# Optimization experiments

Measured on AMD Instinct MI355X. Metric: run time of the kernel, lower is better.

## Reference

```python
import jax, jax.numpy as jnp
import numpy as np

B, N, C, W = 256, 4096, 16, 10
L = N - W + 1
EPS = 1e-5


def setup_inputs() -> dict:
    key = jax.random.key(0)
    ks = jax.random.split(key, 6)
    def lin(k, shape, fan_in):
        # mimic nn.Linear default init scale ~ U(-1/sqrt(fan), 1/sqrt(fan))
        b = 1.0 / np.sqrt(fan_in)
        return jax.random.uniform(k, shape, jnp.float32, -b, b)
    return {
        "x": jax.random.normal(ks[0], (B, N, C, 2), jnp.float32),
        "W_in_real": lin(ks[1], (C, L), L),      # per-channel input filter (real)
        "W_in_imag": lin(ks[2], (C, L), L),      # per-channel input filter (imag)
        "W_nl": lin(ks[3], (C, 2, 2 * C), 2 * C),  # per-channel Linear(2C -> 2)
        "W_out_real": lin(ks[4], (C, W), W),      # per-channel output filter (real)
        "W_out_imag": lin(ks[5], (C, W), W),      # per-channel output filter (imag)
        "gamma": jnp.ones((C,), jnp.float32),     # BatchNorm1d weight
        "beta": jnp.zeros((C,), jnp.float32),     # BatchNorm1d bias
    }


def _depthwise_valid(x_bcn, w_cl):
    # sliding dot-products f[:, c, id] = sum_l x[:, c, id+l] * w[c, l]
    # == depthwise 1D valid correlation: [B,C,N] * [C,L] -> [B,C,W]
    nC = w_cl.shape[0]
    return jax.lax.conv_general_dilated(
        x_bcn, w_cl[:, None, :], window_strides=(1,), padding='VALID',
        dimension_numbers=('NCH', 'OIH', 'NCH'), feature_group_count=nC)


def reference(x, W_in_real, W_in_imag, W_nl, W_out_real, W_out_imag, gamma, beta):
    xr = jnp.transpose(x[..., 0], (0, 2, 1))  # [B,C,N]
    xi = jnp.transpose(x[..., 1], (0, 2, 1))
    # stage 1: per-channel windowed filters + amplitude (|f|^2) scaling
    fr = jnp.transpose(_depthwise_valid(xr, W_in_real), (0, 2, 1))  # [B,W,C]
    fi = jnp.transpose(_depthwise_valid(xi, W_in_imag), (0, 2, 1))  # [B,W,C]
    amp = fr * fr + fi * fi
    fr = amp * fr
    fi = amp * fi
    # stage 2: per-channel nonlin Linear(2C -> 2) on cat([real, imag])
    tf = jnp.concatenate([fr, fi], axis=-1)            # [B,W,2C]
    nl = jnp.einsum('bwi,coi->bwco', tf, W_nl)         # [B,W,C,2]
    nr, ni = nl[..., 0], nl[..., 1]                    # [B,W,C]
    # stage 3: per-channel output filters over the out_window dim
    out_r = jnp.einsum('bwc,cw->bc', nr, W_out_real)   # [B,C]
    out_i = jnp.einsum('bwc,cw->bc', ni, W_out_imag)   # [B,C]
    out = jnp.stack([out_r, out_i], axis=-1)           # [B,C,2]
    # BatchNorm1d(n_channels) in training mode: stats over (batch, last) per channel
    mean = out.mean(axis=(0, 2), keepdims=True)
    var = out.var(axis=(0, 2), keepdims=True)
    return (out - mean) / jnp.sqrt(var + EPS) * gamma[None, :, None] + beta[None, :, None]
```

## Files before the change

### kernel.cpp

```cpp
#include <hip/hip_runtime.h>

#define BB 256
#define NN 4096
#define CC 16
#define WW 10
#define LL 4087
#define EPSF 1e-5f

__global__ __launch_bounds__(256) void pack_weights(const float* __restrict__ Wr,
                                                    const float* __restrict__ Wi,
                                                    float2* __restrict__ pk) {
    int tg = blockIdx.x * 256 + threadIdx.x;
    int n = tg >> 4, c = tg & 15;
    float2 v = make_float2(0.f, 0.f);
    if (n < LL) { v.x = Wr[c * LL + n]; v.y = Wi[c * LL + n]; }
    pk[tg] = v;
}

template <bool PK>
__global__ __launch_bounds__(512, 2) void fused_main(const float* __restrict__ x,
                                                     const float2* __restrict__ pk,
                                                     const float* __restrict__ Wr,
                                                     const float* __restrict__ Wi,
                                                     const float* __restrict__ Wnl,
                                                     const float* __restrict__ Wor,
                                                     const float* __restrict__ Woi,
                                                     float* __restrict__ outraw) {
    const int b = blockIdx.x;
    const int tid = threadIdx.x;
    const int tc = tid >> 4;
    const int c = tid & 15;
    const int n0 = tc * 128;

    const float2* __restrict__ x2 = (const float2*)x + (size_t)b * (NN * CC);

    float wr[16], wi[16];
    float fr[WW], fi[WW];
#pragma unroll
    for (int w = 0; w < WW; ++w) { fr[w] = 0.f; fi[w] = 0.f; }

#pragma unroll
    for (int i = 1; i <= 9; ++i) {
        const int m = n0 - i;
        float vr = 0.f, vi = 0.f;
        if (PK) {
            if (m >= 0) { const float2 t = pk[m * 16 + c]; vr = t.x; vi = t.y; }
        } else {
            const int mc = m < 0 ? 0 : m;
            const float a = Wr[c * LL + mc], q = Wi[c * LL + mc];
            vr = (m >= 0) ? a : 0.f;
            vi = (m >= 0) ? q : 0.f;
        }
        wr[16 - i] = vr;
        wi[16 - i] = vi;
    }

#pragma unroll 1
    for (int g = 0; g < 8; ++g) {
        const int nb = n0 + g * 16;
#pragma unroll
        for (int p = 0; p < 16; ++p) {
            const int n = nb + p;
            float vr, vi;
            if (PK) {
                const float2 t = pk[n * 16 + c];
                vr = t.x; vi = t.y;
            } else {
                const int nc2 = (n < LL) ? n : (LL - 1);
                const float a = Wr[c * LL + nc2], q = Wi[c * LL + nc2];
                vr = (n < LL) ? a : 0.f;
                vi = (n < LL) ? q : 0.f;
            }
            const float2 xv = x2[n * 16 + c];
            wr[p] = vr;
            wi[p] = vi;
#pragma unroll
            for (int w = 0; w < WW; ++w) {
                fr[w] += xv.x * wr[(p - w) & 15];
                fi[w] += xv.y * wi[(p - w) & 15];
            }
        }
    }

#pragma unroll
    for (int w = 0; w < WW; ++w) {
        fr[w] += __shfl_xor(fr[w], 16);
        fr[w] += __shfl_xor(fr[w], 32);
        fi[w] += __shfl_xor(fi[w], 16);
        fi[w] += __shfl_xor(fi[w], 32);
    }
    __shared__ float red[8][320];
    __shared__ float F2[320];
    __shared__ float nls[320];
    const int lane = tid & 63, wave = tid >> 6;
    if (lane < 16) {
#pragma unroll
        for (int w = 0; w < WW; ++w) {
            red[wave][lane * 20 + w] = fr[w];
            red[wave][lane * 20 + 10 + w] = fi[w];
        }
    }
    __syncthreads();
    if (tid < 320) {
        float s = 0.f;
#pragma unroll
        for (int k = 0; k < 8; ++k) s += red[k][tid];
        F2[tid] = s;
    }
    __syncthreads();
    if (tid < 160) {
        const int cc = tid / 10, w = tid % 10;
        const float a = F2[cc * 20 + w], q = F2[cc * 20 + 10 + w];
        const float amp = a * a + q * q;
        F2[cc * 20 + w] = a * amp;
        F2[cc * 20 + 10 + w] = q * amp;
    }
    __syncthreads();
    if (tid < 320) {
        const int cc = tid / 20, rem = tid % 20, o = rem / 10, w = rem % 10;
        const float* __restrict__ wn = Wnl + (cc * 2 + o) * 32;
        float acc = 0.f;
#pragma unroll
        for (int i = 0; i < 16; ++i) acc += F2[i * 20 + w] * wn[i];
#pragma unroll
        for (int i = 0; i < 16; ++i) acc += F2[i * 20 + 10 + w] * wn[16 + i];
        nls[tid] = acc;
    }
    __syncthreads();
    if (tid < 32) {
        const int cc = tid >> 1, o = tid & 1;
        const float* __restrict__ wo = (o == 0 ? Wor : Woi) + cc * WW;
        float acc = 0.f;
#pragma unroll
        for (int w = 0; w < WW; ++w) acc += nls[cc * 20 + o * 10 + w] * wo[w];
        outraw[b * 32 + cc * 2 + o] = acc;
    }
}

__global__ __launch_bounds__(256) void bnorm(float* __restrict__ out,
                                             const float* __restrict__ gamma,
                                             const float* __restrict__ beta) {
    const int c = blockIdx.x;
    const int t = threadIdx.x;
    const float v0 = out[t * 32 + c * 2 + 0];
    const float v1 = out[t * 32 + c * 2 + 1];
    float s = v0 + v1;
    float ss = v0 * v0 + v1 * v1;
#pragma unroll
    for (int off = 32; off > 0; off >>= 1) {
        s += __shfl_down(s, off, 64);
        ss += __shfl_down(ss, off, 64);
    }
    __shared__ float ls[8];
    const int wave = t >> 6, lane = t & 63;
    if (lane == 0) { ls[wave * 2] = s; ls[wave * 2 + 1] = ss; }
    __syncthreads();
    const float S = ls[0] + ls[2] + ls[4] + ls[6];
    const float SS = ls[1] + ls[3] + ls[5] + ls[7];
    const float mean = S * (1.f / 512.f);
    const float var = SS * (1.f / 512.f) - mean * mean;
    const float scale = gamma[c] * rsqrtf(var + EPSF);
    const float sh = beta[c];
    out[t * 32 + c * 2 + 0] = (v0 - mean) * scale + sh;
    out[t * 32 + c * 2 + 1] = (v1 - mean) * scale + sh;
}

extern "C" void kernel_launch(void* const* d_in, const int* in_sizes, int n_in,
                              void* d_out, int out_size, void* d_ws, size_t ws_size,
                              hipStream_t stream) {
    const float* x     = (const float*)d_in[0];
    const float* Wr    = (const float*)d_in[1];
    const float* Wi    = (const float*)d_in[2];
    const float* Wnl   = (const float*)d_in[3];
    const float* Wor   = (const float*)d_in[4];
    const float* Woi   = (const float*)d_in[5];
    const float* gamma = (const float*)d_in[6];
    const float* beta  = (const float*)d_in[7];
    float* out = (float*)d_out;

    const size_t pk_bytes = (size_t)NN * CC * sizeof(float2);
    float2* pk = (float2*)d_ws;
    const bool use_pk = (ws_size >= pk_bytes);

    if (use_pk) {
        hipLaunchKernelGGL(pack_weights, dim3(256), dim3(256), 0, stream, Wr, Wi, pk);
        hipLaunchKernelGGL((fused_main<true>), dim3(BB), dim3(512), 0, stream,
                           x, pk, Wr, Wi, Wnl, Wor, Woi, out);
    } else {
        hipLaunchKernelGGL((fused_main<false>), dim3(BB), dim3(512), 0, stream,
                           x, pk, Wr, Wi, Wnl, Wor, Woi, out);
    }
    hipLaunchKernelGGL(bnorm, dim3(CC), dim3(256), 0, stream, out, gamma, beta);
}
```

Baseline: 213.8 us.

## Process two channels per thread with float4 loads and packed weight layout

Each thread now handles two channels (real and imag for each) and reads x as 16-byte vectors, using nontemporal loads, instead of 8-byte float2. The packed weight buffer is laid out as per-channel-pair float4 rows, so each thread streams contiguous weights. Each thread covers 64 positions instead of 128, which doubles the register accumulators and needs an extra shuffle level in the reduction. The aim is fewer, wider memory transactions on the bandwidth-bound x stream, at the cost of register pressure under launch_bounds(512,2).

```diff
diff --git a/kernel.cpp b/kernel.cpp
--- a/kernel.cpp
+++ b/kernel.cpp
@@ -7,19 +7,27 @@
 #define LL 4087
 #define EPSF 1e-5f
 
+typedef float f4v __attribute__((ext_vector_type(4)));
+
 __global__ __launch_bounds__(256) void pack_weights(const float* __restrict__ Wr,
                                                     const float* __restrict__ Wi,
-                                                    float2* __restrict__ pk) {
-    int tg = blockIdx.x * 256 + threadIdx.x;
-    int n = tg >> 4, c = tg & 15;
-    float2 v = make_float2(0.f, 0.f);
-    if (n < LL) { v.x = Wr[c * LL + n]; v.y = Wi[c * LL + n]; }
-    pk[tg] = v;
+                                                    float4* __restrict__ pk4) {
+    const int q = blockIdx.y;
+    const int n = blockIdx.x * 256 + threadIdx.x;
+    const int c0 = 2 * q, c1 = 2 * q + 1;
+    float4 v = make_float4(0.f, 0.f, 0.f, 0.f);
+    if (n < LL) {
+        v.x = Wr[c0 * LL + n];
+        v.y = Wi[c0 * LL + n];
+        v.z = Wr[c1 * LL + n];
+        v.w = Wi[c1 * LL + n];
+    }
+    pk4[q * NN + n] = v;
 }
 
 template <bool PK>
 __global__ __launch_bounds__(512, 2) void fused_main(const float* __restrict__ x,
-                                                     const float2* __restrict__ pk,
+                                                     const float4* __restrict__ pk4,
                                                      const float* __restrict__ Wr,
                                                      const float* __restrict__ Wi,
                                                      const float* __restrict__ Wnl,
@@ -28,76 +36,85 @@
                                                      float* __restrict__ outraw) {
     const int b = blockIdx.x;
     const int tid = threadIdx.x;
-    const int tc = tid >> 4;
-    const int c = tid & 15;
-    const int n0 = tc * 128;
-
-    const float2* __restrict__ x2 = (const float2*)x + (size_t)b * (NN * CC);
-
-    float wr[16], wi[16];
-    float fr[WW], fi[WW];
-#pragma unroll
-    for (int w = 0; w < WW; ++w) { fr[w] = 0.f; fi[w] = 0.f; }
+    const int tc = tid >> 3;
+    const int q = tid & 7;
+    const int n0 = tc * 64;
+
+    const f4v* __restrict__ x4 = (const f4v*)x + (size_t)b * (NN * 8);
+    const float4* __restrict__ pq = pk4 + q * NN;
+
+    float w0[16], w1[16], w2[16], w3[16];
+    float a0[WW], a1[WW], a2[WW], a3[WW];
+#pragma unroll
+    for (int w = 0; w < WW; ++w) { a0[w] = 0.f; a1[w] = 0.f; a2[w] = 0.f; a3[w] = 0.f; }
 
 #pragma unroll
     for (int i = 1; i <= 9; ++i) {
         const int m = n0 - i;
-        float vr = 0.f, vi = 0.f;
+        float4 wv = make_float4(0.f, 0.f, 0.f, 0.f);
         if (PK) {
-            if (m >= 0) { const float2 t = pk[m * 16 + c]; vr = t.x; vi = t.y; }
+            if (m >= 0) wv = pq[m];
         } else {
             const int mc = m < 0 ? 0 : m;
-            const float a = Wr[c * LL + mc], q = Wi[c * LL + mc];
-            vr = (m >= 0) ? a : 0.f;
-            vi = (m >= 0) ? q : 0.f;
+            const float g = (m >= 0) ? 1.f : 0.f;
+            wv.x = Wr[(2 * q) * LL + mc] * g;
+            wv.y = Wi[(2 * q) * LL + mc] * g;
+            wv.z = Wr[(2 * q + 1) * LL + mc] * g;
+            wv.w = Wi[(2 * q + 1) * LL + mc] * g;
         }
-        wr[16 - i] = vr;
-        wi[16 - i] = vi;
+        const int slot = 16 - i;
+        w0[slot] = wv.x; w1[slot] = wv.y; w2[slot] = wv.z; w3[slot] = wv.w;
     }
 
 #pragma unroll 1
-    for (int g = 0; g < 8; ++g) {
+    for (int g = 0; g < 4; ++g) {
         const int nb = n0 + g * 16;
 #pragma unroll
         for (int p = 0; p < 16; ++p) {
             const int n = nb + p;
-            float vr, vi;
+            float4 wv;
             if (PK) {
-                const float2 t = pk[n * 16 + c];
-                vr = t.x; vi = t.y;
+                wv = pq[n];
             } else {
-                const int nc2 = (n < LL) ? n : (LL - 1);
-                const float a = Wr[c * LL + nc2], q = Wi[c * LL + nc2];
-                vr = (n < LL) ? a : 0.f;
-                vi = (n < LL) ? q : 0.f;
+                const int nc2 = (n < LL) ? n : 0;
+                const float gg = (n < LL) ? 1.f : 0.f;
+                wv.x = Wr[(2 * q) * LL + nc2] * gg;
+                wv.y = Wi[(2 * q) * LL + nc2] * gg;
+                wv.z = Wr[(2 * q + 1) * LL + nc2] * gg;
+                wv.w = Wi[(2 * q + 1) * LL + nc2] * gg;
             }
-            const float2 xv = x2[n * 16 + c];
-            wr[p] = vr;
-            wi[p] = vi;
+            const f4v xv = __builtin_nontemporal_load(&x4[n * 8 + q]);
+            w0[p] = wv.x; w1[p] = wv.y; w2[p] = wv.z; w3[p] = wv.w;
 #pragma unroll
             for (int w = 0; w < WW; ++w) {
-                fr[w] += xv.x * wr[(p - w) & 15];
-                fi[w] += xv.y * wi[(p - w) & 15];
+                const int slot = (p - w) & 15;
+                a0[w] += xv.x * w0[slot];
+                a1[w] += xv.y * w1[slot];
+                a2[w] += xv.z * w2[slot];
+                a3[w] += xv.w * w3[slot];
             }
         }
     }
 
 #pragma unroll
     for (int w = 0; w < WW; ++w) {
-        fr[w] += __shfl_xor(fr[w], 16);
-        fr[w] += __shfl_xor(fr[w], 32);
-        fi[w] += __shfl_xor(fi[w], 16);
-        fi[w] += __shfl_xor(fi[w], 32);
+        a0[w] += __shfl_xor(a0[w], 8);  a0[w] += __shfl_xor(a0[w], 16);  a0[w] += __shfl_xor(a0[w], 32);
+        a1[w] += __shfl_xor(a1[w], 8);  a1[w] += __shfl_xor(a1[w], 16);  a1[w] += __shfl_xor(a1[w], 32);
+        a2[w] += __shfl_xor(a2[w], 8);  a2[w] += __shfl_xor(a2[w], 16);  a2[w] += __shfl_xor(a2[w], 32);
+        a3[w] += __shfl_xor(a3[w], 8);  a3[w] += __shfl_xor(a3[w], 16);  a3[w] += __shfl_xor(a3[w], 32);
     }
     __shared__ float red[8][320];
     __shared__ float F2[320];
     __shared__ float nls[320];
     const int lane = tid & 63, wave = tid >> 6;
-    if (lane < 16) {
+    if (lane < 8) {
+        float* __restrict__ r = &red[wave][q * 40];
 #pragma unroll
         for (int w = 0; w < WW; ++w) {
-            red[wave][lane * 20 + w] = fr[w];
-            red[wave][lane * 20 + 10 + w] = fi[w];
+            r[w] = a0[w];
+            r[10 + w] = a1[w];
+            r[20 + w] = a2[w];
+            r[30 + w] = a3[w];
         }
     }
     __syncthreads();
@@ -110,10 +127,10 @@
     __syncthreads();
     if (tid < 160) {
         const int cc = tid / 10, w = tid % 10;
-        const float a = F2[cc * 20 + w], q = F2[cc * 20 + 10 + w];
-        const float amp = a * a + q * q;
+        const float a = F2[cc * 20 + w], qi = F2[cc * 20 + 10 + w];
+        const float amp = a * a + qi * qi;
         F2[cc * 20 + w] = a * amp;
-        F2[cc * 20 + 10 + w] = q * amp;
+        F2[cc * 20 + 10 + w] = qi * amp;
     }
     __syncthreads();
     if (tid < 320) {
@@ -178,17 +195,17 @@
     const float* beta  = (const float*)d_in[7];
     float* out = (float*)d_out;
 
-    const size_t pk_bytes = (size_t)NN * CC * sizeof(float2);
-    float2* pk = (float2*)d_ws;
+    const size_t pk_bytes = (size_t)8 * NN * sizeof(float4);
+    float4* pk4 = (float4*)d_ws;
     const bool use_pk = (ws_size >= pk_bytes);
 
     if (use_pk) {
-        hipLaunchKernelGGL(pack_weights, dim3(256), dim3(256), 0, stream, Wr, Wi, pk);
+        hipLaunchKernelGGL(pack_weights, dim3(16, 8), dim3(256), 0, stream, Wr, Wi, pk4);
         hipLaunchKernelGGL((fused_main<true>), dim3(BB), dim3(512), 0, stream,
-                           x, pk, Wr, Wi, Wnl, Wor, Woi, out);
+                           x, pk4, Wr, Wi, Wnl, Wor, Woi, out);
     } else {
         hipLaunchKernelGGL((fused_main<false>), dim3(BB), dim3(512), 0, stream,
-                           x, pk, Wr, Wi, Wnl, Wor, Woi, out);
+                           x, pk4, Wr, Wi, Wnl, Wor, Woi, out);
     }
     hipLaunchKernelGGL(bnorm, dim3(CC), dim3(256), 0, stream, out, gamma, beta);
 }
```

Result: slower. 225.4 us (+5.4%).
